# Kernel optimization log

Hardware: AMD Instinct MI355X
Metric: run time of the kernel (lower is better)

The kernel has to match this reference:

```python
import jax, jax.numpy as jnp
import numpy as np

BS, N, DIM, HEADS = 4, 2048, 512, 8
HEAD_DIM = DIM // HEADS
SCALE = HEAD_DIM ** 0.5
NEG = -1000000.0


def setup_inputs() -> dict:
    key = jax.random.key(0)
    ks = jax.random.split(key, 6)
    x = jax.random.normal(ks[0], (BS, N, DIM), dtype=jnp.float32)
    mask = jax.random.randint(ks[1], (BS, N), 0, 2, dtype=jnp.int32)
    s = 1.0 / np.sqrt(DIM)
    Wq = jax.random.normal(ks[2], (DIM, DIM), dtype=jnp.float32) * s
    Wk = jax.random.normal(ks[3], (DIM, DIM), dtype=jnp.float32) * s
    Wv = jax.random.normal(ks[4], (DIM, DIM), dtype=jnp.float32) * s
    Wo = jax.random.normal(ks[5], (DIM, DIM), dtype=jnp.float32) * s
    return {"x": x, "Wq": Wq, "Wk": Wk, "Wv": Wv, "Wo": Wo, "mask": mask}


def reference(x, Wq, Wk, Wv, Wo, mask):
    # q,k,v: (bs, n, dim) -> (bs, h, n, d)
    def split_heads(t):
        return t.reshape(BS, N, HEADS, HEAD_DIM).transpose(0, 2, 1, 3)
    q = split_heads(x @ Wq.T)
    k = split_heads(x @ Wk.T)
    v = split_heads(x @ Wv.T)
    # scores: (bs, h, n, n)
    scores = jnp.einsum('bhqd,bhkd->bhqk', q, k) / SCALE
    # key-padding mask broadcast over heads and query positions
    keep = (mask == 1)[:, None, None, :]  # (bs,1,1,n)
    scores = jnp.where(keep, scores, NEG)
    attn = jax.nn.softmax(scores, axis=-1)
    out = jnp.einsum('bhqk,bhkd->bhqd', attn, v)
    out = out.transpose(0, 2, 1, 3).reshape(BS, N, DIM)
    return out @ Wo.T
```

## Files before the change

kernel.cpp:

```cpp
#include <hip/hip_runtime.h>
#include <hip/hip_bf16.h>

#define BS 4
#define SEQ 2048
#define DIM 512
#define HEADS 8
#define HD 64
#define ROWS (BS*SEQ)
#define SCL2E 0.1803368801111244f
#define NEGB (-1.4426950408889634e6f)

typedef __attribute__((ext_vector_type(8))) short bf16x8;
typedef __attribute__((ext_vector_type(4))) short bf16x4;
typedef __attribute__((ext_vector_type(4))) float floatx4;
typedef unsigned short u16;
typedef unsigned int u32;

__device__ __forceinline__ u16 f2bf(float f) {
    union { float f; unsigned u; } v; v.f = f;
    unsigned r = v.u + 0x7fff + ((v.u >> 16) & 1);
    return (u16)(r >> 16);
}

__device__ __forceinline__ unsigned pack2bf(float a, float b) {
#if __has_builtin(__builtin_amdgcn_cvt_pk_bf16_f32)
    typedef __attribute__((ext_vector_type(2))) __bf16 bf2;
    union { bf2 v; unsigned u; } cv;
    cv.v = __builtin_amdgcn_cvt_pk_bf16_f32(a, b);
    return cv.u;
#else
    return (unsigned)f2bf(a) | ((unsigned)f2bf(b) << 16);
#endif
}

__device__ __forceinline__ float fexp2(float x) {
#if __has_builtin(__builtin_amdgcn_exp2f)
    return __builtin_amdgcn_exp2f(x);
#else
    return __expf(x * 0.6931471805599453f);
#endif
}

__device__ __forceinline__ void gload16(const u16* g, u16* l) {
    __builtin_amdgcn_global_load_lds(
        (const __attribute__((address_space(1))) u32*)g,
        (__attribute__((address_space(3))) u32*)l, 16, 0, 0);
}

__global__ __launch_bounds__(256) void convert_all(
    const float* __restrict__ x, const float* __restrict__ Wq,
    const float* __restrict__ Wk, const float* __restrict__ Wv,
    const float* __restrict__ Wo, const int* __restrict__ mask,
    u16* __restrict__ xb, u16* __restrict__ wqb,
    u16* __restrict__ wkb, u16* __restrict__ wvb,
    u16* __restrict__ wob, float* __restrict__ biasf)
{
    int i = blockIdx.x * 256 + threadIdx.x;
    if (i < 1048576 + 262144) {
        const float* src; u16* dst; int off;
        if (i < 1048576) { src = x; dst = xb; off = i; }
        else {
            int j = i - 1048576; int seg = j >> 16; off = j & 65535;
            src = seg == 0 ? Wq : seg == 1 ? Wk : seg == 2 ? Wv : Wo;
            dst = seg == 0 ? wqb : seg == 1 ? wkb : seg == 2 ? wvb : wob;
        }
        float4 v = ((const float4*)src)[off];
        ushort4 o;
        o.x = f2bf(v.x); o.y = f2bf(v.y); o.z = f2bf(v.z); o.w = f2bf(v.w);
        ((ushort4*)dst)[off] = o;
    } else {
        int jb = i - 1310720;
        int4 mv = ((const int4*)mask)[jb];
        float4 bo;
        bo.x = (mv.x == 1) ? 0.f : NEGB;
        bo.y = (mv.y == 1) ? 0.f : NEGB;
        bo.z = (mv.z == 1) ? 0.f : NEGB;
        bo.w = (mv.w == 1) ? 0.f : NEGB;
        ((float4*)biasf)[jb] = bo;
    }
}

__global__ __launch_bounds__(256, 3) void gemm_qkv_fused(
    const u16* __restrict__ A, const u16* __restrict__ Wcat,
    u16* __restrict__ Oq, u16* __restrict__ Okf, u16* __restrict__ Ovf)
{
    __shared__ u16 ldsA[8192];
    __shared__ u16 ldsB[8192];

    int n0 = blockIdx.x * 128;
    int m0 = blockIdx.y * 128;
    int tid = threadIdx.x;
    int w = tid >> 6, lane = tid & 63, quad = lane >> 4, l16 = lane & 15;
    int mo = (w & 1) * 64, no = (w >> 1) * 64;
    int l7 = l16 & 7;

    int sr = lane >> 3, sc = lane & 7, gc = sc ^ sr;
    const u16* gA0 = A    + (long)(m0 + sr) * DIM + gc * 8;
    const u16* gB0 = Wcat + (long)(n0 + sr) * DIM + gc * 8;

    floatx4 acc[4][4];
    #pragma unroll
    for (int mt = 0; mt < 4; mt++)
        #pragma unroll
        for (int nt = 0; nt < 4; nt++) acc[mt][nt] = (floatx4){0.f,0.f,0.f,0.f};

    for (int k0 = 0; k0 < DIM; k0 += 64) {
        #pragma unroll
        for (int i = 0; i < 4; i++) {
            int ch = w * 4 + i;
            gload16(gA0 + (long)ch * 8 * DIM + k0, &ldsA[ch * 512]);
            gload16(gB0 + (long)ch * 8 * DIM + k0, &ldsB[ch * 512]);
        }
        __syncthreads();

        #pragma unroll
        for (int kc = 0; kc < 2; kc++) {
            int swz = ((kc * 4 + quad) ^ l7) * 8;
            bf16x8 af[4], bf[4];
            #pragma unroll
            for (int t4 = 0; t4 < 4; t4++) {
                af[t4] = *(const bf16x8*)&ldsA[(mo + t4*16 + l16) * 64 + swz];
                bf[t4] = *(const bf16x8*)&ldsB[(no + t4*16 + l16) * 64 + swz];
            }
            #pragma unroll
            for (int mt = 0; mt < 4; mt++)
                #pragma unroll
                for (int nt = 0; nt < 4; nt++)
                    acc[mt][nt] = __builtin_amdgcn_mfma_f32_16x16x32_bf16(
                        af[mt], bf[nt], acc[mt][nt], 0, 0, 0);
        }
        __syncthreads();
    }

    int seg = n0 >> 9;
    if (seg == 0) {
        #pragma unroll
        for (int mt = 0; mt < 4; mt++)
            #pragma unroll
            for (int nt = 0; nt < 4; nt++)
                #pragma unroll
                for (int r = 0; r < 4; r++) {
                    int row = m0 + mo + mt*16 + quad*4 + r;
                    int col9 = (n0 + no + nt*16 + l16) & 511;
                    int b = row >> 11, n = row & 2047, h = col9 >> 6, d = col9 & 63;
                    Oq[(((long)(b * HEADS + h) * SEQ + n) << 6) + d] = f2bf(acc[mt][nt][r]);
                }
    } else if (seg == 1) {
        #pragma unroll
        for (int mt = 0; mt < 4; mt++)
            #pragma unroll
            for (int nt = 0; nt < 4; nt++)
                #pragma unroll
                for (int r = 0; r < 4; r++) {
                    int row = m0 + mo + mt*16 + quad*4 + r;
                    int col9 = (n0 + no + nt*16 + l16) & 511;
                    int b = row >> 11, keyn = row & 2047, h = col9 >> 6, dd = col9 & 63;
                    int kt = keyn >> 6, ntk = (keyn >> 4) & 3, l16k = keyn & 15;
                    int g = dd >> 5, quadk = (dd >> 3) & 3, j = dd & 7;
                    long offv = ((long)((b*HEADS + h)*32 + kt) << 12)
                              + ((ntk*2 + g) << 9) + ((quadk*16 + l16k) << 3) + j;
                    Okf[offv] = f2bf(acc[mt][nt][r] * SCL2E);
                }
    } else {
        #pragma unroll
        for (int mt = 0; mt < 4; mt++)
            #pragma unroll
            for (int nt = 0; nt < 4; nt++) {
                int rowb = m0 + mo + mt*16 + quad*4;
                int col9 = (n0 + no + nt*16 + l16) & 511;
                int b = rowb >> 11, keyn = rowb & 2047, h = col9 >> 6;
                int tile = (keyn >> 6) & 31;
                long offv = ((long)((b*HEADS + h)*32 + tile) << 12)
                          + ((long)(mt >> 1) << 11) + (nt << 9)
                          + ((quad*16 + l16) << 3) + ((mt & 1) << 2);
                ushort4 st;
                st.x = f2bf(acc[mt][nt][0]); st.y = f2bf(acc[mt][nt][1]);
                st.z = f2bf(acc[mt][nt][2]); st.w = f2bf(acc[mt][nt][3]);
                *(ushort4*)&Ovf[offv] = st;
            }
    }
}

__global__ __launch_bounds__(256, 2) void flash_attn(
    const u16* __restrict__ Q, const u16* __restrict__ Kf,
    const u16* __restrict__ Vf, const float* __restrict__ biasf,
    u16* __restrict__ ctx)
{
    __shared__ float red[4352];

    int bx = blockIdx.x;
    int cx = bx & 7, sx = bx >> 3;
    int gg = ((sx >> 5) << 3) | cx;
    int qi = sx & 31;
    int q0 = qi * 64;
    int h  = gg & 7;
    int b  = gg >> 3;
    int bh = b * HEADS + h;

    int tid = threadIdx.x;
    int w = tid >> 6, lane = tid & 63, quad = lane >> 4, l16 = lane & 15;

    bf16x8 qb[4][2];
    #pragma unroll
    for (int nt = 0; nt < 4; nt++) {
        const u16* qp = Q + ((long)bh * SEQ + q0 + nt*16 + l16) * HD + quad * 8;
        qb[nt][0] = *(const bf16x8*)(qp);
        qb[nt][1] = *(const bf16x8*)(qp + 32);
    }

    const u16* Kw = Kf + ((long)bh << 17) + w*2048 + lane*8;
    const u16* Vw = Vf + ((long)bh << 17) + w*2048 + lane*8;
    const float* bw = biasf + b * SEQ + w*32 + quad*4;

    short one_s = (l16 == 0) ? (short)0x3F80 : (short)0;
    bf16x8 ones8 = { one_s, one_s, one_s, one_s, one_s, one_s, one_s, one_s };

    bf16x8 k00 = *(const bf16x8*)(Kw);
    bf16x8 k01 = *(const bf16x8*)(Kw + 512);
    bf16x8 k10 = *(const bf16x8*)(Kw + 1024);
    bf16x8 k11 = *(const bf16x8*)(Kw + 1536);
    bf16x8 vb0 = *(const bf16x8*)(Vw);
    bf16x8 vb1 = *(const bf16x8*)(Vw + 512);
    bf16x8 vb2 = *(const bf16x8*)(Vw + 1024);
    bf16x8 vb3 = *(const bf16x8*)(Vw + 1536);
    float4 bv0 = *(const float4*)(bw);
    float4 bv1 = *(const float4*)(bw + 16);

    floatx4 o[4][4];
    floatx4 o5[4];
    #pragma unroll
    for (int nt = 0; nt < 4; nt++) {
        #pragma unroll
        for (int ct = 0; ct < 4; ct++) o[nt][ct] = (floatx4){0.f,0.f,0.f,0.f};
        o5[nt] = (floatx4){0.f,0.f,0.f,0.f};
    }

    #pragma unroll 2
    for (int it = 0; it < 16; it++) {
        bf16x8 k00n=k00, k01n=k01, k10n=k10, k11n=k11;
        bf16x8 vb0n=vb0, vb1n=vb1, vb2n=vb2, vb3n=vb3;
        float4 bv0n=bv0, bv1n=bv1;
        if (it < 15) {
            const u16* kp = Kw + (long)(it+1)*8192;
            const u16* vp = Vw + (long)(it+1)*8192;
            k00n = *(const bf16x8*)(kp);
            k01n = *(const bf16x8*)(kp + 512);
            k10n = *(const bf16x8*)(kp + 1024);
            k11n = *(const bf16x8*)(kp + 1536);
            vb0n = *(const bf16x8*)(vp);
            vb1n = *(const bf16x8*)(vp + 512);
            vb2n = *(const bf16x8*)(vp + 1024);
            vb3n = *(const bf16x8*)(vp + 1536);
            bv0n = *(const float4*)(bw + (it+1)*128);
            bv1n = *(const float4*)(bw + (it+1)*128 + 16);
        }

        #pragma unroll
        for (int nt = 0; nt < 4; nt++) {
            floatx4 s0, s1;
            s0[0] = bv0.x; s0[1] = bv0.y; s0[2] = bv0.z; s0[3] = bv0.w;
            s1[0] = bv1.x; s1[1] = bv1.y; s1[2] = bv1.z; s1[3] = bv1.w;
            __builtin_amdgcn_s_setprio(1);
            s0 = __builtin_amdgcn_mfma_f32_16x16x32_bf16(k00, qb[nt][0], s0, 0, 0, 0);
            s0 = __builtin_amdgcn_mfma_f32_16x16x32_bf16(k01, qb[nt][1], s0, 0, 0, 0);
            s1 = __builtin_amdgcn_mfma_f32_16x16x32_bf16(k10, qb[nt][0], s1, 0, 0, 0);
            s1 = __builtin_amdgcn_mfma_f32_16x16x32_bf16(k11, qb[nt][1], s1, 0, 0, 0);
            __builtin_amdgcn_s_setprio(0);
            float p0 = fexp2(s0[0]);
            float p1 = fexp2(s0[1]);
            float p2 = fexp2(s0[2]);
            float p3 = fexp2(s0[3]);
            float p4 = fexp2(s1[0]);
            float p5 = fexp2(s1[1]);
            float p6 = fexp2(s1[2]);
            float p7 = fexp2(s1[3]);
            union { bf16x8 v; unsigned u[4]; } pu;
            pu.u[0] = pack2bf(p0, p1);
            pu.u[1] = pack2bf(p2, p3);
            pu.u[2] = pack2bf(p4, p5);
            pu.u[3] = pack2bf(p6, p7);
            __builtin_amdgcn_s_setprio(1);
            o[nt][0] = __builtin_amdgcn_mfma_f32_16x16x32_bf16(pu.v, vb0, o[nt][0], 0, 0, 0);
            o[nt][1] = __builtin_amdgcn_mfma_f32_16x16x32_bf16(pu.v, vb1, o[nt][1], 0, 0, 0);
            o[nt][2] = __builtin_amdgcn_mfma_f32_16x16x32_bf16(pu.v, vb2, o[nt][2], 0, 0, 0);
            o[nt][3] = __builtin_amdgcn_mfma_f32_16x16x32_bf16(pu.v, vb3, o[nt][3], 0, 0, 0);
            o5[nt] = __builtin_amdgcn_mfma_f32_16x16x32_bf16(pu.v, ones8, o5[nt], 0, 0, 0);
            __builtin_amdgcn_s_setprio(0);
        }

        k00 = k00n; k01 = k01n; k10 = k10n; k11 = k11n;
        vb0 = vb0n; vb1 = vb1n; vb2 = vb2n; vb3 = vb3n;
        bv0 = bv0n; bv1 = bv1n;
    }

    __syncthreads();
    float* ldsf = red;
    floatx4* ldsv = (floatx4*)red;

    if (l16 == 0) {
        #pragma unroll
        for (int nt = 0; nt < 4; nt++)
            #pragma unroll
            for (int r = 0; r < 4; r++)
                ldsf[4096 + w*64 + nt*16 + quad*4 + r] = o5[nt][r];
    }
    __syncthreads();

    #pragma unroll
    for (int i2 = 1; i2 < 4; i2++) {
        int tslot = (w + i2) & 3;
        #pragma unroll
        for (int nt = 0; nt < 4; nt++)
            if (nt == tslot) {
                #pragma unroll
                for (int ct = 0; ct < 4; ct++)
                    ldsv[nt*256 + ct*64 + lane] = o[nt][ct];
            }
        __syncthreads();
        #pragma unroll
        for (int nt = 0; nt < 4; nt++)
            if (nt == w) {
                #pragma unroll
                for (int ct = 0; ct < 4; ct++) {
                    floatx4 v = ldsv[nt*256 + ct*64 + lane];
                    o[nt][ct] += v;
                }
            }
        __syncthreads();
    }

    #pragma unroll
    for (int nt = 0; nt < 4; nt++) {
        if (nt != w) continue;
        float inv[4];
        #pragma unroll
        for (int r = 0; r < 4; r++) {
            int q = w*16 + quad*4 + r;
            float sden = ldsf[4096 + q] + ldsf[4096 + 64 + q]
                       + ldsf[4096 + 128 + q] + ldsf[4096 + 192 + q];
            inv[r] = 1.0f / sden;
        }
        #pragma unroll
        for (int ct = 0; ct < 4; ct++) {
            int col = h * HD + ct*16 + l16;
            long rb = (long)(b * SEQ + q0 + w*16 + quad*4);
            #pragma unroll
            for (int r = 0; r < 4; r++)
                ctx[(rb + r) * DIM + col] = f2bf(o[nt][ct][r] * inv[r]);
        }
    }
}

__global__ __launch_bounds__(256, 4) void gemm_proj(
    const u16* __restrict__ A, const u16* __restrict__ Bt,
    float* __restrict__ Out)
{
    __shared__ u16 ldsA[4096];
    __shared__ u16 ldsB[8192];

    int n0 = blockIdx.x * 128;
    int m0 = blockIdx.y * 64;
    int tid = threadIdx.x;
    int w = tid >> 6, lane = tid & 63, quad = lane >> 4, l16 = lane & 15;
    int l7 = l16 & 7;

    int sr = lane >> 3, sc = lane & 7, gc = sc ^ sr;
    const u16* gA0 = A  + (long)(m0 + sr) * DIM + gc * 8;
    const u16* gB0 = Bt + (long)(n0 + sr) * DIM + gc * 8;

    floatx4 acc[8];
    #pragma unroll
    for (int nt = 0; nt < 8; nt++) acc[nt] = (floatx4){0.f,0.f,0.f,0.f};

    for (int k0 = 0; k0 < DIM; k0 += 64) {
        gload16(gA0 + (long)(2*w)   * 8 * DIM + k0, &ldsA[(2*w)   * 512]);
        gload16(gA0 + (long)(2*w+1) * 8 * DIM + k0, &ldsA[(2*w+1) * 512]);
        #pragma unroll
        for (int i = 0; i < 4; i++)
            gload16(gB0 + (long)(4*w+i) * 8 * DIM + k0, &ldsB[(4*w+i) * 512]);
        __syncthreads();

        #pragma unroll
        for (int kc = 0; kc < 2; kc++) {
            int swz = ((kc * 4 + quad) ^ l7) * 8;
            bf16x8 af = *(const bf16x8*)&ldsA[(w*16 + l16) * 64 + swz];
            #pragma unroll
            for (int nt = 0; nt < 8; nt++) {
                bf16x8 bfv = *(const bf16x8*)&ldsB[(nt*16 + l16) * 64 + swz];
                acc[nt] = __builtin_amdgcn_mfma_f32_16x16x32_bf16(
                    af, bfv, acc[nt], 0, 0, 0);
            }
        }
        __syncthreads();
    }

    #pragma unroll
    for (int nt = 0; nt < 8; nt++)
        #pragma unroll
        for (int r = 0; r < 4; r++) {
            int row = m0 + w*16 + quad*4 + r;
            int col = n0 + nt*16 + l16;
            Out[(long)row * DIM + col] = acc[nt][r];
        }
}

extern "C" void kernel_launch(void* const* d_in, const int* in_sizes, int n_in,
                              void* d_out, int out_size, void* d_ws, size_t ws_size,
                              hipStream_t stream) {
    const float* x  = (const float*)d_in[0];
    const float* Wq = (const float*)d_in[1];
    const float* Wk = (const float*)d_in[2];
    const float* Wv = (const float*)d_in[3];
    const float* Wo = (const float*)d_in[4];
    const int* mask = (const int*)d_in[5];
    float* out = (float*)d_out;

    char* ws = (char*)d_ws;
    size_t off = 0;
    u16* xb  = (u16*)(ws + off); off += (size_t)ROWS * DIM * 2;
    u16* wqb = (u16*)(ws + off); off += (size_t)DIM * DIM * 2;
    u16* wkb = (u16*)(ws + off); off += (size_t)DIM * DIM * 2;
    u16* wvb = (u16*)(ws + off); off += (size_t)DIM * DIM * 2;
    u16* wob = (u16*)(ws + off); off += (size_t)DIM * DIM * 2;
    u16* Qh  = (u16*)(ws + off); off += (size_t)ROWS * DIM * 2;
    u16* Kfr = (u16*)(ws + off); off += (size_t)ROWS * DIM * 2;
    u16* Vfr = (u16*)(ws + off); off += (size_t)ROWS * DIM * 2;
    u16* ctx = (u16*)(ws + off); off += (size_t)ROWS * DIM * 2;
    float* biasf = (float*)(ws + off); off += (size_t)BS * SEQ * 4;

    convert_all<<<5128, 256, 0, stream>>>(x, Wq, Wk, Wv, Wo, mask,
                                          xb, wqb, wkb, wvb, wob, biasf);
    gemm_qkv_fused<<<dim3(12, 64), 256, 0, stream>>>(xb, wqb, Qh, Kfr, Vfr);
    flash_attn<<<BS * HEADS * (SEQ / 64), 256, 0, stream>>>(Qh, Kfr, Vfr, biasf, ctx);
    gemm_proj<<<dim3(4, 128), 256, 0, stream>>>(ctx, wob, out);

    (void)in_sizes; (void)n_in; (void)out_size; (void)ws_size;
}
```

Before: 161.0 us.

## Replace ones-MFMA row sum with VALU accumulation and batch MFMA phases

The softmax denominator was computed with an extra MFMA against a ones vector. It is now accumulated as a per-lane float sum of the exponentials and reduced across quads with shuffles after the loop. The loop body is also regrouped so all four QK tiles' MFMAs issue first, then all exps, then all PV MFMAs. This cuts one MFMA out of five per tile and gives the scheduler more independent work, at the cost of higher register pressure. The sum now uses fp32 exponentials rather than their bf16-rounded values.

```diff
diff --git a/kernel.cpp b/kernel.cpp
--- a/kernel.cpp
+++ b/kernel.cpp
@@ -212,9 +212,6 @@
     const u16* Vw = Vf + ((long)bh << 17) + w*2048 + lane*8;
     const float* bw = biasf + b * SEQ + w*32 + quad*4;
 
-    short one_s = (l16 == 0) ? (short)0x3F80 : (short)0;
-    bf16x8 ones8 = { one_s, one_s, one_s, one_s, one_s, one_s, one_s, one_s };
-
     bf16x8 k00 = *(const bf16x8*)(Kw);
     bf16x8 k01 = *(const bf16x8*)(Kw + 512);
     bf16x8 k10 = *(const bf16x8*)(Kw + 1024);
@@ -227,12 +224,12 @@
     float4 bv1 = *(const float4*)(bw + 16);
 
     floatx4 o[4][4];
-    floatx4 o5[4];
+    float lsum[4];
     #pragma unroll
     for (int nt = 0; nt < 4; nt++) {
         #pragma unroll
         for (int ct = 0; ct < 4; ct++) o[nt][ct] = (floatx4){0.f,0.f,0.f,0.f};
-        o5[nt] = (floatx4){0.f,0.f,0.f,0.f};
+        lsum[nt] = 0.f;
     }
 
     #pragma unroll 2
@@ -255,54 +252,69 @@
             bv1n = *(const float4*)(bw + (it+1)*128 + 16);
         }
 
+        floatx4 sA[4], sB[4];
+        __builtin_amdgcn_s_setprio(1);
         #pragma unroll
         for (int nt = 0; nt < 4; nt++) {
-            floatx4 s0, s1;
-            s0[0] = bv0.x; s0[1] = bv0.y; s0[2] = bv0.z; s0[3] = bv0.w;
-            s1[0] = bv1.x; s1[1] = bv1.y; s1[2] = bv1.z; s1[3] = bv1.w;
-            __builtin_amdgcn_s_setprio(1);
-            s0 = __builtin_amdgcn_mfma_f32_16x16x32_bf16(k00, qb[nt][0], s0, 0, 0, 0);
-            s0 = __builtin_amdgcn_mfma_f32_16x16x32_bf16(k01, qb[nt][1], s0, 0, 0, 0);
-            s1 = __builtin_amdgcn_mfma_f32_16x16x32_bf16(k10, qb[nt][0], s1, 0, 0, 0);
-            s1 = __builtin_amdgcn_mfma_f32_16x16x32_bf16(k11, qb[nt][1], s1, 0, 0, 0);
-            __builtin_amdgcn_s_setprio(0);
-            float p0 = fexp2(s0[0]);
-            float p1 = fexp2(s0[1]);
-            float p2 = fexp2(s0[2]);
-            float p3 = fexp2(s0[3]);
-            float p4 = fexp2(s1[0]);
-            float p5 = fexp2(s1[1]);
-            float p6 = fexp2(s1[2]);
-            float p7 = fexp2(s1[3]);
-            union { bf16x8 v; unsigned u[4]; } pu;
-            pu.u[0] = pack2bf(p0, p1);
-            pu.u[1] = pack2bf(p2, p3);
-            pu.u[2] = pack2bf(p4, p5);
-            pu.u[3] = pack2bf(p6, p7);
-            __builtin_amdgcn_s_setprio(1);
-            o[nt][0] = __builtin_amdgcn_mfma_f32_16x16x32_bf16(pu.v, vb0, o[nt][0], 0, 0, 0);
-            o[nt][1] = __builtin_amdgcn_mfma_f32_16x16x32_bf16(pu.v, vb1, o[nt][1], 0, 0, 0);
-            o[nt][2] = __builtin_amdgcn_mfma_f32_16x16x32_bf16(pu.v, vb2, o[nt][2], 0, 0, 0);
-            o[nt][3] = __builtin_amdgcn_mfma_f32_16x16x32_bf16(pu.v, vb3, o[nt][3], 0, 0, 0);
-            o5[nt] = __builtin_amdgcn_mfma_f32_16x16x32_bf16(pu.v, ones8, o5[nt], 0, 0, 0);
-            __builtin_amdgcn_s_setprio(0);
-        }
+            floatx4 t0, t1;
+            t0[0] = bv0.x; t0[1] = bv0.y; t0[2] = bv0.z; t0[3] = bv0.w;
+            t1[0] = bv1.x; t1[1] = bv1.y; t1[2] = bv1.z; t1[3] = bv1.w;
+            t0 = __builtin_amdgcn_mfma_f32_16x16x32_bf16(k00, qb[nt][0], t0, 0, 0, 0);
+            t0 = __builtin_amdgcn_mfma_f32_16x16x32_bf16(k01, qb[nt][1], t0, 0, 0, 0);
+            t1 = __builtin_amdgcn_mfma_f32_16x16x32_bf16(k10, qb[nt][0], t1, 0, 0, 0);
+            t1 = __builtin_amdgcn_mfma_f32_16x16x32_bf16(k11, qb[nt][1], t1, 0, 0, 0);
+            sA[nt] = t0; sB[nt] = t1;
+        }
+        __builtin_amdgcn_s_setprio(0);
+
+        union PU { bf16x8 v; unsigned u[4]; };
+        PU pu[4];
+        #pragma unroll
+        for (int nt = 0; nt < 4; nt++) {
+            float p0 = fexp2(sA[nt][0]);
+            float p1 = fexp2(sA[nt][1]);
+            float p2 = fexp2(sA[nt][2]);
+            float p3 = fexp2(sA[nt][3]);
+            float p4 = fexp2(sB[nt][0]);
+            float p5 = fexp2(sB[nt][1]);
+            float p6 = fexp2(sB[nt][2]);
+            float p7 = fexp2(sB[nt][3]);
+            pu[nt].u[0] = pack2bf(p0, p1);
+            pu[nt].u[1] = pack2bf(p2, p3);
+            pu[nt].u[2] = pack2bf(p4, p5);
+            pu[nt].u[3] = pack2bf(p6, p7);
+            lsum[nt] += ((p0 + p1) + (p2 + p3)) + ((p4 + p5) + (p6 + p7));
+        }
+
+        __builtin_amdgcn_s_setprio(1);
+        #pragma unroll
+        for (int nt = 0; nt < 4; nt++) {
+            o[nt][0] = __builtin_amdgcn_mfma_f32_16x16x32_bf16(pu[nt].v, vb0, o[nt][0], 0, 0, 0);
+            o[nt][1] = __builtin_amdgcn_mfma_f32_16x16x32_bf16(pu[nt].v, vb1, o[nt][1], 0, 0, 0);
+            o[nt][2] = __builtin_amdgcn_mfma_f32_16x16x32_bf16(pu[nt].v, vb2, o[nt][2], 0, 0, 0);
+            o[nt][3] = __builtin_amdgcn_mfma_f32_16x16x32_bf16(pu[nt].v, vb3, o[nt][3], 0, 0, 0);
+        }
+        __builtin_amdgcn_s_setprio(0);
 
         k00 = k00n; k01 = k01n; k10 = k10n; k11 = k11n;
         vb0 = vb0n; vb1 = vb1n; vb2 = vb2n; vb3 = vb3n;
         bv0 = bv0n; bv1 = bv1n;
     }
 
+    #pragma unroll
+    for (int nt = 0; nt < 4; nt++) {
+        lsum[nt] += __shfl_xor(lsum[nt], 16);
+        lsum[nt] += __shfl_xor(lsum[nt], 32);
+    }
+
     __syncthreads();
     float* ldsf = red;
     floatx4* ldsv = (floatx4*)red;
 
-    if (l16 == 0) {
+    if (quad == 0) {
         #pragma unroll
         for (int nt = 0; nt < 4; nt++)
-            #pragma unroll
-            for (int r = 0; r < 4; r++)
-                ldsf[4096 + w*64 + nt*16 + quad*4 + r] = o5[nt][r];
+            ldsf[4096 + w*64 + nt*16 + l16] = lsum[nt];
     }
     __syncthreads();
 
```

Result: no change. 164.2 us (+2.0%).

## Raise occupancy by cutting V/bias prefetch and replacing ones-MFMA row sums

Applied to the files above, without the earlier changes.

Raises the launch-bounds target from 2 to 3 blocks per SM and lowers register pressure to fit it. V and bias are now loaded inside the current iteration instead of being double-buffered, and the bias is added after the QK MFMA rather than seeding its accumulator. The row-sum MFMA against a ones vector is replaced by scalar adds on the probabilities followed by a cross-lane shuffle reduction. The cost is that V loads are no longer prefetched and their latency is exposed, relying on the extra waves per SM to hide it.

```diff
diff --git a/kernel.cpp b/kernel.cpp
--- a/kernel.cpp
+++ b/kernel.cpp
@@ -181,7 +181,7 @@
     }
 }
 
-__global__ __launch_bounds__(256, 2) void flash_attn(
+__global__ __launch_bounds__(256, 3) void flash_attn(
     const u16* __restrict__ Q, const u16* __restrict__ Kf,
     const u16* __restrict__ Vf, const float* __restrict__ biasf,
     u16* __restrict__ ctx)
@@ -212,97 +212,89 @@
     const u16* Vw = Vf + ((long)bh << 17) + w*2048 + lane*8;
     const float* bw = biasf + b * SEQ + w*32 + quad*4;
 
-    short one_s = (l16 == 0) ? (short)0x3F80 : (short)0;
-    bf16x8 ones8 = { one_s, one_s, one_s, one_s, one_s, one_s, one_s, one_s };
+    const floatx4 zeroq = (floatx4){0.f, 0.f, 0.f, 0.f};
 
     bf16x8 k00 = *(const bf16x8*)(Kw);
     bf16x8 k01 = *(const bf16x8*)(Kw + 512);
     bf16x8 k10 = *(const bf16x8*)(Kw + 1024);
     bf16x8 k11 = *(const bf16x8*)(Kw + 1536);
-    bf16x8 vb0 = *(const bf16x8*)(Vw);
-    bf16x8 vb1 = *(const bf16x8*)(Vw + 512);
-    bf16x8 vb2 = *(const bf16x8*)(Vw + 1024);
-    bf16x8 vb3 = *(const bf16x8*)(Vw + 1536);
-    float4 bv0 = *(const float4*)(bw);
-    float4 bv1 = *(const float4*)(bw + 16);
 
     floatx4 o[4][4];
-    floatx4 o5[4];
+    float lsum[4];
     #pragma unroll
     for (int nt = 0; nt < 4; nt++) {
         #pragma unroll
         for (int ct = 0; ct < 4; ct++) o[nt][ct] = (floatx4){0.f,0.f,0.f,0.f};
-        o5[nt] = (floatx4){0.f,0.f,0.f,0.f};
+        lsum[nt] = 0.f;
     }
 
     #pragma unroll 2
     for (int it = 0; it < 16; it++) {
+        const u16* vp = Vw + (long)it*8192;
+        bf16x8 vb0 = *(const bf16x8*)(vp);
+        bf16x8 vb1 = *(const bf16x8*)(vp + 512);
+        bf16x8 vb2 = *(const bf16x8*)(vp + 1024);
+        bf16x8 vb3 = *(const bf16x8*)(vp + 1536);
+        float4 bv0 = *(const float4*)(bw + it*128);
+        float4 bv1 = *(const float4*)(bw + it*128 + 16);
+
         bf16x8 k00n=k00, k01n=k01, k10n=k10, k11n=k11;
-        bf16x8 vb0n=vb0, vb1n=vb1, vb2n=vb2, vb3n=vb3;
-        float4 bv0n=bv0, bv1n=bv1;
         if (it < 15) {
             const u16* kp = Kw + (long)(it+1)*8192;
-            const u16* vp = Vw + (long)(it+1)*8192;
             k00n = *(const bf16x8*)(kp);
             k01n = *(const bf16x8*)(kp + 512);
             k10n = *(const bf16x8*)(kp + 1024);
             k11n = *(const bf16x8*)(kp + 1536);
-            vb0n = *(const bf16x8*)(vp);
-            vb1n = *(const bf16x8*)(vp + 512);
-            vb2n = *(const bf16x8*)(vp + 1024);
-            vb3n = *(const bf16x8*)(vp + 1536);
-            bv0n = *(const float4*)(bw + (it+1)*128);
-            bv1n = *(const float4*)(bw + (it+1)*128 + 16);
         }
 
         #pragma unroll
         for (int nt = 0; nt < 4; nt++) {
             floatx4 s0, s1;
-            s0[0] = bv0.x; s0[1] = bv0.y; s0[2] = bv0.z; s0[3] = bv0.w;
-            s1[0] = bv1.x; s1[1] = bv1.y; s1[2] = bv1.z; s1[3] = bv1.w;
             __builtin_amdgcn_s_setprio(1);
-            s0 = __builtin_amdgcn_mfma_f32_16x16x32_bf16(k00, qb[nt][0], s0, 0, 0, 0);
+            s0 = __builtin_amdgcn_mfma_f32_16x16x32_bf16(k00, qb[nt][0], zeroq, 0, 0, 0);
             s0 = __builtin_amdgcn_mfma_f32_16x16x32_bf16(k01, qb[nt][1], s0, 0, 0, 0);
-            s1 = __builtin_amdgcn_mfma_f32_16x16x32_bf16(k10, qb[nt][0], s1, 0, 0, 0);
+            s1 = __builtin_amdgcn_mfma_f32_16x16x32_bf16(k10, qb[nt][0], zeroq, 0, 0, 0);
             s1 = __builtin_amdgcn_mfma_f32_16x16x32_bf16(k11, qb[nt][1], s1, 0, 0, 0);
             __builtin_amdgcn_s_setprio(0);
-            float p0 = fexp2(s0[0]);
-            float p1 = fexp2(s0[1]);
-            float p2 = fexp2(s0[2]);
-            float p3 = fexp2(s0[3]);
-            float p4 = fexp2(s1[0]);
-            float p5 = fexp2(s1[1]);
-            float p6 = fexp2(s1[2]);
-            float p7 = fexp2(s1[3]);
+            float p0 = fexp2(s0[0] + bv0.x);
+            float p1 = fexp2(s0[1] + bv0.y);
+            float p2 = fexp2(s0[2] + bv0.z);
+            float p3 = fexp2(s0[3] + bv0.w);
+            float p4 = fexp2(s1[0] + bv1.x);
+            float p5 = fexp2(s1[1] + bv1.y);
+            float p6 = fexp2(s1[2] + bv1.z);
+            float p7 = fexp2(s1[3] + bv1.w);
             union { bf16x8 v; unsigned u[4]; } pu;
             pu.u[0] = pack2bf(p0, p1);
             pu.u[1] = pack2bf(p2, p3);
             pu.u[2] = pack2bf(p4, p5);
             pu.u[3] = pack2bf(p6, p7);
+            lsum[nt] += ((p0 + p1) + (p2 + p3)) + ((p4 + p5) + (p6 + p7));
             __builtin_amdgcn_s_setprio(1);
             o[nt][0] = __builtin_amdgcn_mfma_f32_16x16x32_bf16(pu.v, vb0, o[nt][0], 0, 0, 0);
             o[nt][1] = __builtin_amdgcn_mfma_f32_16x16x32_bf16(pu.v, vb1, o[nt][1], 0, 0, 0);
             o[nt][2] = __builtin_amdgcn_mfma_f32_16x16x32_bf16(pu.v, vb2, o[nt][2], 0, 0, 0);
             o[nt][3] = __builtin_amdgcn_mfma_f32_16x16x32_bf16(pu.v, vb3, o[nt][3], 0, 0, 0);
-            o5[nt] = __builtin_amdgcn_mfma_f32_16x16x32_bf16(pu.v, ones8, o5[nt], 0, 0, 0);
             __builtin_amdgcn_s_setprio(0);
         }
 
         k00 = k00n; k01 = k01n; k10 = k10n; k11 = k11n;
-        vb0 = vb0n; vb1 = vb1n; vb2 = vb2n; vb3 = vb3n;
-        bv0 = bv0n; bv1 = bv1n;
+    }
+
+    #pragma unroll
+    for (int nt = 0; nt < 4; nt++) {
+        lsum[nt] += __shfl_xor(lsum[nt], 16);
+        lsum[nt] += __shfl_xor(lsum[nt], 32);
     }
 
     __syncthreads();
     float* ldsf = red;
     floatx4* ldsv = (floatx4*)red;
 
-    if (l16 == 0) {
+    if (quad == 0) {
         #pragma unroll
         for (int nt = 0; nt < 4; nt++)
-            #pragma unroll
-            for (int r = 0; r < 4; r++)
-                ldsf[4096 + w*64 + nt*16 + quad*4 + r] = o5[nt][r];
+            ldsf[4096 + w*64 + nt*16 + l16] = lsum[nt];
     }
     __syncthreads();
 
```

After: 392.8 us. 2.44x slower.
